# Kernel tuning notes

Hardware: AMD Instinct MI355X
Metric: run time of the kernel (lower is better)

Reference implementation:

```python
import jax, jax.numpy as jnp
import numpy as np

H = 64  # hidden_size
I = 8   # input_size
O = 1   # output_size


def setup_inputs() -> dict:
    key = jax.random.key(0)
    ks = jax.random.split(key, 7)
    B, T = 4096, 512
    s_ih = 1.0 / np.sqrt(H)
    inp = {
        "x": jax.random.normal(ks[0], (B, T, I), dtype=jnp.float32),
        # PyTorch LSTM params: W_ih [4H, I], W_hh [4H, H], biases [4H] (gate order i,f,g,o)
        "W_ih": jax.random.uniform(ks[1], (4 * H, I), jnp.float32, -s_ih, s_ih),
        "W_hh": jax.random.uniform(ks[2], (4 * H, H), jnp.float32, -s_ih, s_ih),
        "b_ih": jax.random.uniform(ks[3], (4 * H,), jnp.float32, -s_ih, s_ih),
        "b_hh": jax.random.uniform(ks[4], (4 * H,), jnp.float32, -s_ih, s_ih),
        "W_fc": jax.random.uniform(ks[5], (O, H), jnp.float32, -s_ih, s_ih),
        "b_fc": jax.random.uniform(ks[6], (O,), jnp.float32, -s_ih, s_ih),
    }
    return inp


def _lstm_last_h(x, W_ih, W_hh, b_ih, b_hh):
    B, T, _ = x.shape
    # Precompute input contributions for all timesteps: [T, B, 4H]
    xg = jnp.einsum("bti,gi->tbg", x, W_ih) + (b_ih + b_hh)

    def step(carry, xg_t):
        h, c = carry
        gates = xg_t + h @ W_hh.T  # [B, 4H]
        i, f, g, o = jnp.split(gates, 4, axis=-1)  # torch gate order i,f,g,o
        i = jax.nn.sigmoid(i)
        f = jax.nn.sigmoid(f)
        g = jnp.tanh(g)
        o = jax.nn.sigmoid(o)
        c = f * c + i * g
        h = o * jnp.tanh(c)
        return (h, c), None

    h0 = jnp.zeros((B, H), x.dtype)
    c0 = jnp.zeros((B, H), x.dtype)
    (h_T, _), _ = jax.lax.scan(step, (h0, c0), xg)
    return h_T  # [B, H] == out[:, -1, :]


def reference(x, W_ih, W_hh, b_ih, b_hh, W_fc, b_fc):
    h_T = _lstm_last_h(x, W_ih, W_hh, b_ih, b_hh)
    return h_T @ W_fc.T + b_fc  # [B, O]
```

## Files before the change

### kernel.cpp

```cpp
#include <hip/hip_runtime.h>

#define HSZ 64
#define ISZ 8
#define TSZ 512
#define BTILE 16
#define NW 16
#define KP 104

typedef _Float16 f16;
typedef __attribute__((ext_vector_type(8))) _Float16 f16x8;
typedef __attribute__((ext_vector_type(4))) float f32x4;
typedef unsigned short u16;

__device__ __forceinline__ u16 f16bits(float f) {
    union { f16 h; u16 u; } v; v.h = (f16)f;
    return v.u;
}

__global__ __launch_bounds__(1024, 4) void lstm_w16b(
    const float* __restrict__ x,
    const float* __restrict__ W_ih,
    const float* __restrict__ W_hh,
    const float* __restrict__ b_ih,
    const float* __restrict__ b_hh,
    const float* __restrict__ W_fc,
    const float* __restrict__ b_fc,
    float* __restrict__ out)
{
    const int tid = threadIdx.x;
    const int w  = tid >> 6;
    const int l  = tid & 63;
    const int lr = l & 15;
    const int lg = l >> 4;
    const int B0 = blockIdx.x * BTILE;
    const int hcol = 4 * w + lg;

    __shared__ __align__(16) u16 H[2][BTILE][KP];
    __shared__ float red[NW][BTILE];

    for (int i = tid; i < 2 * BTILE * KP; i += 1024)
        ((u16*)H)[i] = 0;

    const int gate = lr & 3;
    const int gc   = gate * HSZ + 4 * w + (lr >> 2);
    const float sc = (gate == 2) ? -2.885390082f : -1.442695041f;
    f16x8 wa0, wa1, wa2;
    {
        const float4 a = *reinterpret_cast<const float4*>(&W_hh[gc * HSZ + lg * 8]);
        const float4 b = *reinterpret_cast<const float4*>(&W_hh[gc * HSZ + lg * 8 + 4]);
        wa0[0] = (f16)(sc * a.x); wa0[1] = (f16)(sc * a.y);
        wa0[2] = (f16)(sc * a.z); wa0[3] = (f16)(sc * a.w);
        wa0[4] = (f16)(sc * b.x); wa0[5] = (f16)(sc * b.y);
        wa0[6] = (f16)(sc * b.z); wa0[7] = (f16)(sc * b.w);
    }
    {
        const float4 a = *reinterpret_cast<const float4*>(&W_hh[gc * HSZ + 32 + lg * 8]);
        const float4 b = *reinterpret_cast<const float4*>(&W_hh[gc * HSZ + 32 + lg * 8 + 4]);
        wa1[0] = (f16)(sc * a.x); wa1[1] = (f16)(sc * a.y);
        wa1[2] = (f16)(sc * a.z); wa1[3] = (f16)(sc * a.w);
        wa1[4] = (f16)(sc * b.x); wa1[5] = (f16)(sc * b.y);
        wa1[6] = (f16)(sc * b.z); wa1[7] = (f16)(sc * b.w);
    }
#pragma unroll
    for (int j = 0; j < 8; ++j) wa2[j] = (f16)0.0f;
    if (lg == 0) {
        const float4 a = *reinterpret_cast<const float4*>(&W_ih[gc * ISZ]);
        const float4 b = *reinterpret_cast<const float4*>(&W_ih[gc * ISZ + 4]);
        wa2[0] = (f16)(sc * a.x); wa2[1] = (f16)(sc * a.y);
        wa2[2] = (f16)(sc * a.z); wa2[3] = (f16)(sc * a.w);
        wa2[4] = (f16)(sc * b.x); wa2[5] = (f16)(sc * b.y);
        wa2[6] = (f16)(sc * b.z); wa2[7] = (f16)(sc * b.w);
    }

    f32x4 bias4;
#pragma unroll
    for (int r = 0; r < 4; ++r) {
        const float s = (r == 2) ? -2.885390082f : -1.442695041f;
        bias4[r] = s * (b_ih[r * HSZ + hcol] + b_hh[r * HSZ + hcol]);
    }

    __syncthreads();

    const float* xptr = x + (size_t)(B0 + w) * TSZ * ISZ + l;
    if (l < 8)
        H[0][w][HSZ + l] = f16bits(xptr[0]);
    __syncthreads();

    const u16* rd0 = &H[0][lr][lg * 8];
    const u16* rd1 = &H[1][lr][lg * 8];
    u16* wr0 = &H[0][lr][hcol];
    u16* wr1 = &H[1][lr][hcol];
    u16* xs0 = &H[0][w][HSZ + l];
    u16* xs1 = &H[1][w][HSZ + l];

    float c = 0.0f, h = 0.0f;
    const float L2 = 2.885390082f;

#define STEP(RD, WR, XS, XIDX, XGUARD)                                           \
    {                                                                            \
        float xv = 0.0f;                                                         \
        if ((l < 8) && (XGUARD))                                                 \
            xv = xptr[(size_t)(XIDX) * ISZ];                                     \
        const f16x8 b0 = *reinterpret_cast<const f16x8*>(RD);                    \
        const f16x8 b1 = *reinterpret_cast<const f16x8*>(RD + 32);               \
        const f16x8 b2 = *reinterpret_cast<const f16x8*>(RD + 64);               \
        f32x4 acc = __builtin_amdgcn_mfma_f32_16x16x32_f16(wa2, b2, bias4, 0, 0, 0); \
        acc = __builtin_amdgcn_mfma_f32_16x16x32_f16(wa0, b0, acc, 0, 0, 0);     \
        acc = __builtin_amdgcn_mfma_f32_16x16x32_f16(wa1, b1, acc, 0, 0, 0);     \
        const float ea = __builtin_amdgcn_exp2f(acc[0]);                         \
        const float eb = __builtin_amdgcn_exp2f(acc[1]);                         \
        const float ed = __builtin_amdgcn_exp2f(acc[2]);                         \
        const float es = __builtin_amdgcn_exp2f(acc[3]);                         \
        const float A1 = 1.0f + ea, B1 = 1.0f + eb, D1 = 1.0f + ed;              \
        const float R1 = __builtin_amdgcn_rcpf(A1 * B1 * D1);                    \
        c = fmaf(c * A1, D1, (1.0f - ed) * B1) * R1;                             \
        const float eu = __builtin_amdgcn_exp2f(-L2 * c);                        \
        const float R2 = __builtin_amdgcn_rcpf((1.0f + es) * (1.0f + eu));       \
        h = (1.0f - eu) * R2;                                                    \
        *(WR) = f16bits(h);                                                      \
        if ((l < 8) && (XGUARD))                                                 \
            *(XS) = f16bits(xv);                                                 \
        __syncthreads();                                                         \
    }

    for (int t = 0; t < TSZ; t += 2) {
        STEP(rd0, wr1, xs1, t + 1, true)
        STEP(rd1, wr0, xs0, t + 2, t < TSZ - 2)
    }
#undef STEP

    float v = h * W_fc[hcol];
    v += __shfl_xor(v, 16);
    v += __shfl_xor(v, 32);
    if (lg == 0) red[w][lr] = v;
    __syncthreads();
    if (tid < BTILE) {
        float s = b_fc[0];
#pragma unroll
        for (int ww = 0; ww < NW; ++ww) s += red[ww][tid];
        out[B0 + tid] = s;
    }
}

extern "C" void kernel_launch(void* const* d_in, const int* in_sizes, int n_in,
                              void* d_out, int out_size, void* d_ws, size_t ws_size,
                              hipStream_t stream) {
    const float* x    = (const float*)d_in[0];
    const float* W_ih = (const float*)d_in[1];
    const float* W_hh = (const float*)d_in[2];
    const float* b_ih = (const float*)d_in[3];
    const float* b_hh = (const float*)d_in[4];
    const float* W_fc = (const float*)d_in[5];
    const float* b_fc = (const float*)d_in[6];
    float* out = (float*)d_out;

    const int B = in_sizes[0] / (TSZ * ISZ);
    lstm_w16b<<<B / BTILE, NW * 64, 0, stream>>>(x, W_ih, W_hh, b_ih, b_hh, W_fc, b_fc, out);
}
```

Before: 253.5 us.

## Halve batch tile and give each wave two hidden-column MFMA chains

Each block now handles 8 batch rows with 8 waves instead of 16 rows with 16 waves, and each wave computes two groups of hidden columns, running two interleaved MFMA accumulation chains and two activation passes per step. The aim is to shrink the per-step barrier to fewer waves and gain instruction-level parallelism from the independent chains, while launching twice as many blocks. The cost is that half of each 16-wide MFMA batch dimension is now unused padding, so total matrix work per useful row doubles. The x-input load is also moved onto wave 0.

```diff
diff --git a/kernel.cpp b/kernel.cpp
--- a/kernel.cpp
+++ b/kernel.cpp
@@ -3,8 +3,8 @@
 #define HSZ 64
 #define ISZ 8
 #define TSZ 512
-#define BTILE 16
-#define NW 16
+#define BTILE 8
+#define NW 8
 #define KP 104
 
 typedef _Float16 f16;
@@ -17,7 +17,7 @@
     return v.u;
 }
 
-__global__ __launch_bounds__(1024, 4) void lstm_w16b(
+__global__ __launch_bounds__(512, 4) void lstm_dual(
     const float* __restrict__ x,
     const float* __restrict__ W_ih,
     const float* __restrict__ W_hh,
@@ -33,103 +33,120 @@
     const int lr = l & 15;
     const int lg = l >> 4;
     const int B0 = blockIdx.x * BTILE;
-    const int hcol = 4 * w + lg;
 
-    __shared__ __align__(16) u16 H[2][BTILE][KP];
-    __shared__ float red[NW][BTILE];
+    __shared__ __align__(16) u16 H[2][16][KP];
+    __shared__ float red[NW][16];
 
-    for (int i = tid; i < 2 * BTILE * KP; i += 1024)
+    for (int i = tid; i < 2 * 16 * KP; i += 512)
         ((u16*)H)[i] = 0;
 
     const int gate = lr & 3;
-    const int gc   = gate * HSZ + 4 * w + (lr >> 2);
     const float sc = (gate == 2) ? -2.885390082f : -1.442695041f;
-    f16x8 wa0, wa1, wa2;
-    {
-        const float4 a = *reinterpret_cast<const float4*>(&W_hh[gc * HSZ + lg * 8]);
-        const float4 b = *reinterpret_cast<const float4*>(&W_hh[gc * HSZ + lg * 8 + 4]);
-        wa0[0] = (f16)(sc * a.x); wa0[1] = (f16)(sc * a.y);
-        wa0[2] = (f16)(sc * a.z); wa0[3] = (f16)(sc * a.w);
-        wa0[4] = (f16)(sc * b.x); wa0[5] = (f16)(sc * b.y);
-        wa0[6] = (f16)(sc * b.z); wa0[7] = (f16)(sc * b.w);
-    }
-    {
-        const float4 a = *reinterpret_cast<const float4*>(&W_hh[gc * HSZ + 32 + lg * 8]);
-        const float4 b = *reinterpret_cast<const float4*>(&W_hh[gc * HSZ + 32 + lg * 8 + 4]);
-        wa1[0] = (f16)(sc * a.x); wa1[1] = (f16)(sc * a.y);
-        wa1[2] = (f16)(sc * a.z); wa1[3] = (f16)(sc * a.w);
-        wa1[4] = (f16)(sc * b.x); wa1[5] = (f16)(sc * b.y);
-        wa1[6] = (f16)(sc * b.z); wa1[7] = (f16)(sc * b.w);
-    }
+    f16x8 wa0[2], wa1[2], wa2[2];
+    f32x4 bias4[2];
 #pragma unroll
-    for (int j = 0; j < 8; ++j) wa2[j] = (f16)0.0f;
-    if (lg == 0) {
-        const float4 a = *reinterpret_cast<const float4*>(&W_ih[gc * ISZ]);
-        const float4 b = *reinterpret_cast<const float4*>(&W_ih[gc * ISZ + 4]);
-        wa2[0] = (f16)(sc * a.x); wa2[1] = (f16)(sc * a.y);
-        wa2[2] = (f16)(sc * a.z); wa2[3] = (f16)(sc * a.w);
-        wa2[4] = (f16)(sc * b.x); wa2[5] = (f16)(sc * b.y);
-        wa2[6] = (f16)(sc * b.z); wa2[7] = (f16)(sc * b.w);
-    }
-
-    f32x4 bias4;
+    for (int q = 0; q < 2; ++q) {
+        const int n  = 2 * w + q;
+        const int gc = gate * HSZ + 4 * n + (lr >> 2);
+        {
+            const float4 a = *reinterpret_cast<const float4*>(&W_hh[gc * HSZ + lg * 8]);
+            const float4 b = *reinterpret_cast<const float4*>(&W_hh[gc * HSZ + lg * 8 + 4]);
+            wa0[q][0] = (f16)(sc * a.x); wa0[q][1] = (f16)(sc * a.y);
+            wa0[q][2] = (f16)(sc * a.z); wa0[q][3] = (f16)(sc * a.w);
+            wa0[q][4] = (f16)(sc * b.x); wa0[q][5] = (f16)(sc * b.y);
+            wa0[q][6] = (f16)(sc * b.z); wa0[q][7] = (f16)(sc * b.w);
+        }
+        {
+            const float4 a = *reinterpret_cast<const float4*>(&W_hh[gc * HSZ + 32 + lg * 8]);
+            const float4 b = *reinterpret_cast<const float4*>(&W_hh[gc * HSZ + 32 + lg * 8 + 4]);
+            wa1[q][0] = (f16)(sc * a.x); wa1[q][1] = (f16)(sc * a.y);
+            wa1[q][2] = (f16)(sc * a.z); wa1[q][3] = (f16)(sc * a.w);
+            wa1[q][4] = (f16)(sc * b.x); wa1[q][5] = (f16)(sc * b.y);
+            wa1[q][6] = (f16)(sc * b.z); wa1[q][7] = (f16)(sc * b.w);
+        }
 #pragma unroll
-    for (int r = 0; r < 4; ++r) {
-        const float s = (r == 2) ? -2.885390082f : -1.442695041f;
-        bias4[r] = s * (b_ih[r * HSZ + hcol] + b_hh[r * HSZ + hcol]);
+        for (int j = 0; j < 8; ++j) wa2[q][j] = (f16)0.0f;
+        if (lg == 0) {
+            const float4 a = *reinterpret_cast<const float4*>(&W_ih[gc * ISZ]);
+            const float4 b = *reinterpret_cast<const float4*>(&W_ih[gc * ISZ + 4]);
+            wa2[q][0] = (f16)(sc * a.x); wa2[q][1] = (f16)(sc * a.y);
+            wa2[q][2] = (f16)(sc * a.z); wa2[q][3] = (f16)(sc * a.w);
+            wa2[q][4] = (f16)(sc * b.x); wa2[q][5] = (f16)(sc * b.y);
+            wa2[q][6] = (f16)(sc * b.z); wa2[q][7] = (f16)(sc * b.w);
+        }
+        const int hc = 4 * n + lg;
+#pragma unroll
+        for (int r = 0; r < 4; ++r) {
+            const float s = (r == 2) ? -2.885390082f : -1.442695041f;
+            bias4[q][r] = s * (b_ih[r * HSZ + hc] + b_hh[r * HSZ + hc]);
+        }
     }
 
     __syncthreads();
 
-    const float* xptr = x + (size_t)(B0 + w) * TSZ * ISZ + l;
-    if (l < 8)
-        H[0][w][HSZ + l] = f16bits(xptr[0]);
+    const float* xptr = x + (size_t)(B0 + (l >> 3)) * TSZ * ISZ + (l & 7);
+    if (w == 0)
+        H[0][l >> 3][HSZ + (l & 7)] = f16bits(xptr[0]);
     __syncthreads();
 
     const u16* rd0 = &H[0][lr][lg * 8];
     const u16* rd1 = &H[1][lr][lg * 8];
-    u16* wr0 = &H[0][lr][hcol];
-    u16* wr1 = &H[1][lr][hcol];
-    u16* xs0 = &H[0][w][HSZ + l];
-    u16* xs1 = &H[1][w][HSZ + l];
+    const int hcol0 = 8 * w + lg, hcol1 = 8 * w + 4 + lg;
+    u16* wrA0 = &H[0][lr][hcol0];  u16* wrA1 = &H[0][lr][hcol1];
+    u16* wrB0 = &H[1][lr][hcol0];  u16* wrB1 = &H[1][lr][hcol1];
+    u16* xsA  = &H[0][l >> 3][HSZ + (l & 7)];
+    u16* xsB  = &H[1][l >> 3][HSZ + (l & 7)];
 
-    float c = 0.0f, h = 0.0f;
+    float c0 = 0.f, c1 = 0.f, h0 = 0.f, h1 = 0.f;
     const float L2 = 2.885390082f;
 
-#define STEP(RD, WR, XS, XIDX, XGUARD)                                           \
-    {                                                                            \
-        float xv = 0.0f;                                                         \
-        if ((l < 8) && (XGUARD))                                                 \
-            xv = xptr[(size_t)(XIDX) * ISZ];                                     \
-        const f16x8 b0 = *reinterpret_cast<const f16x8*>(RD);                    \
-        const f16x8 b1 = *reinterpret_cast<const f16x8*>(RD + 32);               \
-        const f16x8 b2 = *reinterpret_cast<const f16x8*>(RD + 64);               \
-        f32x4 acc = __builtin_amdgcn_mfma_f32_16x16x32_f16(wa2, b2, bias4, 0, 0, 0); \
-        acc = __builtin_amdgcn_mfma_f32_16x16x32_f16(wa0, b0, acc, 0, 0, 0);     \
-        acc = __builtin_amdgcn_mfma_f32_16x16x32_f16(wa1, b1, acc, 0, 0, 0);     \
-        const float ea = __builtin_amdgcn_exp2f(acc[0]);                         \
-        const float eb = __builtin_amdgcn_exp2f(acc[1]);                         \
-        const float ed = __builtin_amdgcn_exp2f(acc[2]);                         \
-        const float es = __builtin_amdgcn_exp2f(acc[3]);                         \
-        const float A1 = 1.0f + ea, B1 = 1.0f + eb, D1 = 1.0f + ed;              \
-        const float R1 = __builtin_amdgcn_rcpf(A1 * B1 * D1);                    \
-        c = fmaf(c * A1, D1, (1.0f - ed) * B1) * R1;                             \
-        const float eu = __builtin_amdgcn_exp2f(-L2 * c);                        \
-        const float R2 = __builtin_amdgcn_rcpf((1.0f + es) * (1.0f + eu));       \
-        h = (1.0f - eu) * R2;                                                    \
-        *(WR) = f16bits(h);                                                      \
-        if ((l < 8) && (XGUARD))                                                 \
-            *(XS) = f16bits(xv);                                                 \
-        __syncthreads();                                                         \
+#define ACT(ACC, CC, HH)                                                       \
+    {                                                                          \
+        const float ea = __builtin_amdgcn_exp2f((ACC)[0]);                     \
+        const float eb = __builtin_amdgcn_exp2f((ACC)[1]);                     \
+        const float ed = __builtin_amdgcn_exp2f((ACC)[2]);                     \
+        const float es = __builtin_amdgcn_exp2f((ACC)[3]);                     \
+        const float A1 = 1.0f + ea, B1 = 1.0f + eb, D1 = 1.0f + ed;            \
+        const float R1 = __builtin_amdgcn_rcpf(A1 * B1 * D1);                  \
+        CC = fmaf(CC * A1, D1, (1.0f - ed) * B1) * R1;                         \
+        const float eu = __builtin_amdgcn_exp2f(-L2 * CC);                     \
+        const float R2 = __builtin_amdgcn_rcpf((1.0f + es) * (1.0f + eu));     \
+        HH = (1.0f - eu) * R2;                                                 \
+    }
+
+#define STEP(RD, WR0, WR1, XS, XIDX, XGUARD)                                   \
+    {                                                                          \
+        float xv = 0.0f;                                                       \
+        if ((w == 0) && (XGUARD))                                              \
+            xv = xptr[(size_t)(XIDX) * ISZ];                                   \
+        const f16x8 b0 = *reinterpret_cast<const f16x8*>(RD);                  \
+        const f16x8 b1 = *reinterpret_cast<const f16x8*>(RD + 32);             \
+        f16x8 b2 = {};                                                         \
+        if (lg == 0)                                                           \
+            b2 = *reinterpret_cast<const f16x8*>(RD + 64);                     \
+        f32x4 a0 = __builtin_amdgcn_mfma_f32_16x16x32_f16(wa2[0], b2, bias4[0], 0, 0, 0); \
+        f32x4 a1 = __builtin_amdgcn_mfma_f32_16x16x32_f16(wa2[1], b2, bias4[1], 0, 0, 0); \
+        a0 = __builtin_amdgcn_mfma_f32_16x16x32_f16(wa0[0], b0, a0, 0, 0, 0);  \
+        a1 = __builtin_amdgcn_mfma_f32_16x16x32_f16(wa0[1], b0, a1, 0, 0, 0);  \
+        a0 = __builtin_amdgcn_mfma_f32_16x16x32_f16(wa1[0], b1, a0, 0, 0, 0);  \
+        a1 = __builtin_amdgcn_mfma_f32_16x16x32_f16(wa1[1], b1, a1, 0, 0, 0);  \
+        ACT(a0, c0, h0)                                                        \
+        ACT(a1, c1, h1)                                                        \
+        *(WR0) = f16bits(h0);                                                  \
+        *(WR1) = f16bits(h1);                                                  \
+        if ((w == 0) && (XGUARD))                                              \
+            *(XS) = f16bits(xv);                                               \
+        __syncthreads();                                                       \
     }
 
     for (int t = 0; t < TSZ; t += 2) {
-        STEP(rd0, wr1, xs1, t + 1, true)
-        STEP(rd1, wr0, xs0, t + 2, t < TSZ - 2)
+        STEP(rd0, wrB0, wrB1, xsB, t + 1, true)
+        STEP(rd1, wrA0, wrA1, xsA, t + 2, t < TSZ - 2)
     }
 #undef STEP
+#undef ACT
 
-    float v = h * W_fc[hcol];
+    float v = h0 * W_fc[hcol0] + h1 * W_fc[hcol1];
     v += __shfl_xor(v, 16);
     v += __shfl_xor(v, 32);
     if (lg == 0) red[w][lr] = v;
@@ -155,5 +172,5 @@
     float* out = (float*)d_out;
 
     const int B = in_sizes[0] / (TSZ * ISZ);
-    lstm_w16b<<<B / BTILE, NW * 64, 0, stream>>>(x, W_ih, W_hh, b_ih, b_hh, W_fc, b_fc, out);
+    lstm_dual<<<B / BTILE, NW * 64, 0, stream>>>(x, W_ih, W_hh, b_ih, b_hh, W_fc, b_fc, out);
 }
```

Measured after the change: 315.2 us. 24.3% more time.

## Load x directly into MFMA B-operand registers and use a raw LDS barrier

Applied to the files above, without the earlier changes.

Instead of staging each timestep's input in shared memory through 8 lanes and reading it back as the third MFMA B operand, every lane now loads its batch row's 8 inputs straight from global memory into registers, one step ahead. It converts them to f16 in place, which lets the shared h buffer shrink its row padding. The __syncthreads is replaced by an explicit lgkmcnt wait plus s_barrier and a sched_barrier, so the barrier does not wait on outstanding global loads. The cost is 16x redundant global loads of x per block (served by cache) and a global-load latency that must be hidden within one step.

```diff
diff --git a/kernel.cpp b/kernel.cpp
--- a/kernel.cpp
+++ b/kernel.cpp
@@ -5,7 +5,7 @@
 #define TSZ 512
 #define BTILE 16
 #define NW 16
-#define KP 104
+#define KP 72
 
 typedef _Float16 f16;
 typedef __attribute__((ext_vector_type(8))) _Float16 f16x8;
@@ -17,7 +17,7 @@
     return v.u;
 }
 
-__global__ __launch_bounds__(1024, 4) void lstm_w16b(
+__global__ __launch_bounds__(1024, 4) void lstm_w16c(
     const float* __restrict__ x,
     const float* __restrict__ W_ih,
     const float* __restrict__ W_hh,
@@ -81,51 +81,54 @@
 
     __syncthreads();
 
-    const float* xptr = x + (size_t)(B0 + w) * TSZ * ISZ + l;
-    if (l < 8)
-        H[0][w][HSZ + l] = f16bits(xptr[0]);
-    __syncthreads();
-
     const u16* rd0 = &H[0][lr][lg * 8];
     const u16* rd1 = &H[1][lr][lg * 8];
     u16* wr0 = &H[0][lr][hcol];
     u16* wr1 = &H[1][lr][hcol];
-    u16* xs0 = &H[0][w][HSZ + l];
-    u16* xs1 = &H[1][w][HSZ + l];
+
+    const float* xrow = x + (size_t)(B0 + lr) * TSZ * ISZ;
+    float4 xa = *reinterpret_cast<const float4*>(xrow);
+    float4 xb = *reinterpret_cast<const float4*>(xrow + 4);
 
     float c = 0.0f, h = 0.0f;
     const float L2 = 2.885390082f;
 
-#define STEP(RD, WR, XS, XIDX, XGUARD)                                           \
-    {                                                                            \
-        float xv = 0.0f;                                                         \
-        if ((l < 8) && (XGUARD))                                                 \
-            xv = xptr[(size_t)(XIDX) * ISZ];                                     \
-        const f16x8 b0 = *reinterpret_cast<const f16x8*>(RD);                    \
-        const f16x8 b1 = *reinterpret_cast<const f16x8*>(RD + 32);               \
-        const f16x8 b2 = *reinterpret_cast<const f16x8*>(RD + 64);               \
+#define STEP(RD, WR, T, GUARD)                                                 \
+    {                                                                          \
+        f16x8 b2;                                                              \
+        b2[0] = (f16)xa.x; b2[1] = (f16)xa.y; b2[2] = (f16)xa.z;               \
+        b2[3] = (f16)xa.w; b2[4] = (f16)xb.x; b2[5] = (f16)xb.y;               \
+        b2[6] = (f16)xb.z; b2[7] = (f16)xb.w;                                  \
+        if (GUARD) {  \
+            xa = *reinterpret_cast<const float4*>(xrow + (size_t)(T + 1) * ISZ);     \
+            xb = *reinterpret_cast<const float4*>(xrow + (size_t)(T + 1) * ISZ + 4); \
+        }                                                                      \
+        const f16x8 b0 = *reinterpret_cast<const f16x8*>(RD);                  \
+        const f16x8 b1 = *reinterpret_cast<const f16x8*>(RD + 32);             \
         f32x4 acc = __builtin_amdgcn_mfma_f32_16x16x32_f16(wa2, b2, bias4, 0, 0, 0); \
-        acc = __builtin_amdgcn_mfma_f32_16x16x32_f16(wa0, b0, acc, 0, 0, 0);     \
-        acc = __builtin_amdgcn_mfma_f32_16x16x32_f16(wa1, b1, acc, 0, 0, 0);     \
-        const float ea = __builtin_amdgcn_exp2f(acc[0]);                         \
-        const float eb = __builtin_amdgcn_exp2f(acc[1]);                         \
-        const float ed = __builtin_amdgcn_exp2f(acc[2]);                         \
-        const float es = __builtin_amdgcn_exp2f(acc[3]);                         \
-        const float A1 = 1.0f + ea, B1 = 1.0f + eb, D1 = 1.0f + ed;              \
-        const float R1 = __builtin_amdgcn_rcpf(A1 * B1 * D1);                    \
-        c = fmaf(c * A1, D1, (1.0f - ed) * B1) * R1;                             \
-        const float eu = __builtin_amdgcn_exp2f(-L2 * c);                        \
-        const float R2 = __builtin_amdgcn_rcpf((1.0f + es) * (1.0f + eu));       \
-        h = (1.0f - eu) * R2;                                                    \
-        *(WR) = f16bits(h);                                                      \
-        if ((l < 8) && (XGUARD))                                                 \
-            *(XS) = f16bits(xv);                                                 \
-        __syncthreads();                                                         \
+        acc = __builtin_amdgcn_mfma_f32_16x16x32_f16(wa0, b0, acc, 0, 0, 0);   \
+        acc = __builtin_amdgcn_mfma_f32_16x16x32_f16(wa1, b1, acc, 0, 0, 0);   \
+        const float ea = __builtin_amdgcn_exp2f(acc[0]);                       \
+        const float eb = __builtin_amdgcn_exp2f(acc[1]);                       \
+        const float ed = __builtin_amdgcn_exp2f(acc[2]);                       \
+        const float es = __builtin_amdgcn_exp2f(acc[3]);                       \
+        const float A1 = 1.0f + ea, B1 = 1.0f + eb, D1 = 1.0f + ed;            \
+        const float R1 = __builtin_amdgcn_rcpf(A1 * B1 * D1);                  \
+        c = fmaf(c * A1, D1, (1.0f - ed) * B1) * R1;                           \
+        const float eu = __builtin_amdgcn_exp2f(-L2 * c);                      \
+        const float R2 = __builtin_amdgcn_rcpf((1.0f + es) * (1.0f + eu));     \
+        h = (1.0f - eu) * R2;                                                  \
+        *(WR) = f16bits(h);                                                    \
+        \
+        asm volatile("s_waitcnt lgkmcnt(0)" ::: "memory");                     \
+        __builtin_amdgcn_s_barrier();                                          \
+        asm volatile("" ::: "memory");                                         \
+        __builtin_amdgcn_sched_barrier(0);                                     \
     }
 
     for (int t = 0; t < TSZ; t += 2) {
-        STEP(rd0, wr1, xs1, t + 1, true)
-        STEP(rd1, wr0, xs0, t + 2, t < TSZ - 2)
+        STEP(rd0, wr1, t, true)
+        STEP(rd1, wr0, t + 1, t < TSZ - 2)
     }
 #undef STEP
 
@@ -155,5 +158,5 @@
     float* out = (float*)d_out;
 
     const int B = in_sizes[0] / (TSZ * ISZ);
-    lstm_w16b<<<B / BTILE, NW * 64, 0, stream>>>(x, W_ih, W_hh, b_ih, b_hh, W_fc, b_fc, out);
+    lstm_w16c<<<B / BTILE, NW * 64, 0, stream>>>(x, W_ih, W_hh, b_ih, b_hh, W_fc, b_fc, out);
 }
```

After: 454.2 us. +79.1%, slower.
